# Kernel optimization log

Hardware: AMD Instinct MI355X
Metric: run time of the kernel (lower is better)

Reference implementation:

```python
import jax, jax.numpy as jnp
import numpy as np

B, I, H, OH = 16384, 256, 256, 64
N_STEPS = 8  # fixed-step dopri5 (adaptive step control replaced by fixed grid for jit)


def setup_inputs() -> dict:
    key = jax.random.key(0)
    ks = jax.random.split(key, 12)
    sH = 1.0 / np.sqrt(H)
    sOH = 1.0 / np.sqrt(OH)
    u = lambda k, shape, s: jax.random.uniform(k, shape, jnp.float32, -s, s)
    return {
        "input": jax.random.normal(ks[0], (B, I), jnp.float32),
        "h_prev": jax.random.normal(ks[1], (B, H), jnp.float32),
        "c_prev": jax.random.normal(ks[2], (B, H), jnp.float32),
        "timespans": jax.random.uniform(ks[3], (B,), jnp.float32, 0.05, 1.0),
        # LSTMCell params (PyTorch layout: gates stacked as [i, f, g, o])
        "W_ih": u(ks[4], (4 * H, I), sH),
        "W_hh": u(ks[5], (4 * H, H), sH),
        "b_ih": u(ks[6], (4 * H,), sH),
        "b_hh": u(ks[7], (4 * H,), sH),
        # ode_func: Linear(H, OH) -> Tanh -> Linear(OH, H)
        "W1": u(ks[8], (OH, H), sH),
        "b1": u(ks[9], (OH,), sH),
        "W2": u(ks[10], (H, OH), sOH),
        "b2": u(ks[11], (H,), sOH),
    }


def reference(input, h_prev, c_prev, timespans, W_ih, W_hh, b_ih, b_hh, W1, b1, W2, b2):
    # --- LSTMCell ---
    gates = input @ W_ih.T + b_ih + h_prev @ W_hh.T + b_hh  # (B, 4H)
    gi, gf, gg, go = jnp.split(gates, 4, axis=-1)
    i = jax.nn.sigmoid(gi)
    f = jax.nn.sigmoid(gf)
    g = jnp.tanh(gg)
    o = jax.nn.sigmoid(go)
    c = f * c_prev + i * g
    h = o * jnp.tanh(c)

    # --- Neural ODE: dy/dt = MLP(y), autonomous, Dormand-Prince RK45 ---
    def ode_f(y):
        return jnp.tanh(y @ W1.T + b1) @ W2.T + b2

    dt = (timespans / N_STEPS)[:, None]  # (B, 1) per-sample step size

    def dopri5_step(y, _):
        k1 = ode_f(y)
        k2 = ode_f(y + dt * (1.0 / 5.0 * k1))
        k3 = ode_f(y + dt * (3.0 / 40.0 * k1 + 9.0 / 40.0 * k2))
        k4 = ode_f(y + dt * (44.0 / 45.0 * k1 - 56.0 / 15.0 * k2 + 32.0 / 9.0 * k3))
        k5 = ode_f(y + dt * (19372.0 / 6561.0 * k1 - 25360.0 / 2187.0 * k2
                             + 64448.0 / 6561.0 * k3 - 212.0 / 729.0 * k4))
        k6 = ode_f(y + dt * (9017.0 / 3168.0 * k1 - 355.0 / 33.0 * k2
                             + 46732.0 / 5247.0 * k3 + 49.0 / 176.0 * k4
                             - 5103.0 / 18656.0 * k5))
        y_next = y + dt * (35.0 / 384.0 * k1 + 500.0 / 1113.0 * k3 + 125.0 / 192.0 * k4
                           - 2187.0 / 6784.0 * k5 + 11.0 / 84.0 * k6)
        return y_next, None

    h_ode, _ = jax.lax.scan(dopri5_step, h, None, length=N_STEPS)
    return h_ode, c
```

## Files before the change

### kernel.cpp

```cpp
#include <hip/hip_runtime.h>
#include <hip/hip_bf16.h>


#define B_N 16384
#define H_N 256

typedef __attribute__((ext_vector_type(8))) short short8;
typedef __attribute__((ext_vector_type(4))) unsigned short u16x4;
typedef __attribute__((ext_vector_type(4))) float f32x4;

__device__ __forceinline__ unsigned short f2bf_s(float x) {
  __hip_bfloat16 h = __float2bfloat16(x);
  return *reinterpret_cast<unsigned short*>(&h);
}

__device__ __forceinline__ short8 pack8f(const float* p) {
  const f32x4 a = *(const f32x4*)p;
  const f32x4 b = *(const f32x4*)(p + 4);
  short8 r;
  r[0] = (short)f2bf_s(a[0]); r[1] = (short)f2bf_s(a[1]);
  r[2] = (short)f2bf_s(a[2]); r[3] = (short)f2bf_s(a[3]);
  r[4] = (short)f2bf_s(b[0]); r[5] = (short)f2bf_s(b[1]);
  r[6] = (short)f2bf_s(b[2]); r[7] = (short)f2bf_s(b[3]);
  return r;
}

__device__ __forceinline__ short8 pack8v(f32x4 a, f32x4 b) {
  short8 r;
  r[0] = (short)f2bf_s(a[0]); r[1] = (short)f2bf_s(a[1]);
  r[2] = (short)f2bf_s(a[2]); r[3] = (short)f2bf_s(a[3]);
  r[4] = (short)f2bf_s(b[0]); r[5] = (short)f2bf_s(b[1]);
  r[6] = (short)f2bf_s(b[2]); r[7] = (short)f2bf_s(b[3]);
  return r;
}

__device__ __forceinline__ float fast_sigmoid(float x) {
  return __builtin_amdgcn_rcpf(1.f + __expf(-x));
}
__device__ __forceinline__ float fast_tanh(float x) {
  float e = __expf(2.f * x);
  return 1.f - 2.f * __builtin_amdgcn_rcpf(e + 1.f);
}

__device__ __forceinline__ void gl_lds16(const void* g, void* l) {
  __builtin_amdgcn_global_load_lds(
      (const __attribute__((address_space(1))) void*)g,
      (__attribute__((address_space(3))) void*)l, 16, 0, 0);
}

__global__ __launch_bounds__(256) void prep_kernel(
    const float* __restrict__ Wih, const float* __restrict__ Whh,
    const float* __restrict__ W1, const float* __restrict__ W2,
    const float* __restrict__ b2,
    unsigned short* __restrict__ wsB, unsigned short* __restrict__ wcB,
    float* __restrict__ uF, unsigned short* __restrict__ w1B,
    unsigned short* __restrict__ w2B) {
  const int bx = blockIdx.x;
  if (bx < 256) {
    int idx = bx * 256 + threadIdx.x;
    int n = idx >> 6, c = idx & 63, k = c * 8;
    const float* src = (k < 256) ? (Wih + (size_t)n * 256 + k)
                                 : (Whh + (size_t)n * 256 + (k - 256));
    *(short8*)(wsB + (size_t)n * 512 + k) = pack8f(src);
  } else if (bx < 272) {
    int idx = (bx - 256) * 256 + threadIdx.x;
    int f = idx >> 6, o = idx & 63;
    float a0 = 0.f, a1 = 0.f, a2 = 0.f, a3 = 0.f;
    for (int h = 0; h < 256; h += 4) {
      a0 = fmaf(W1[f * 256 + h],     W2[h * 64 + o],        a0);
      a1 = fmaf(W1[f * 256 + h + 1], W2[(h + 1) * 64 + o],  a1);
      a2 = fmaf(W1[f * 256 + h + 2], W2[(h + 2) * 64 + o],  a2);
      a3 = fmaf(W1[f * 256 + h + 3], W2[(h + 3) * 64 + o],  a3);
    }
    wcB[f * 64 + o] = f2bf_s((a0 + a1) + (a2 + a3));
  } else if (bx == 272) {
    int f = threadIdx.x;
    if (f < 64) {
      float a0 = 0.f, a1 = 0.f, a2 = 0.f, a3 = 0.f;
      for (int h = 0; h < 256; h += 4) {
        a0 = fmaf(W1[f * 256 + h],     b2[h],     a0);
        a1 = fmaf(W1[f * 256 + h + 1], b2[h + 1], a1);
        a2 = fmaf(W1[f * 256 + h + 2], b2[h + 2], a2);
        a3 = fmaf(W1[f * 256 + h + 3], b2[h + 3], a3);
      }
      uF[f] = (a0 + a1) + (a2 + a3);
    }
  } else if (bx < 281) {
    int idx = (bx - 273) * 256 + threadIdx.x;
    *(short8*)(w1B + (size_t)idx * 8) = pack8f(W1 + (size_t)idx * 8);
  } else {
    int idx = (bx - 281) * 256 + threadIdx.x;
    *(short8*)(w2B + (size_t)idx * 8) = pack8f(W2 + (size_t)idx * 8);
  }
}

__global__ __launch_bounds__(512, 4) void lstm_kernel(
    const float* __restrict__ x, const float* __restrict__ hp,
    const float* __restrict__ cp, const unsigned short* __restrict__ wsB,
    const float* __restrict__ bih, const float* __restrict__ bhh,
    float* __restrict__ out) {
  __shared__ __align__(16) unsigned short Abf[2][128 * 32];
  __shared__ __align__(16) unsigned short Bbf[2][256 * 32];

  const int tid = threadIdx.x;
  const int lane = tid & 63;
  const int wv = tid >> 6;
  const int rg = wv >> 2;
  const int cg = wv & 3;
  const int s = lane & 15, q = lane >> 4;
  const int mb = blockIdx.x * 128;
  const int hb = blockIdx.y;

  f32x4 acc[4][4];
#pragma unroll
  for (int mt = 0; mt < 4; ++mt)
#pragma unroll
    for (int g = 0; g < 4; ++g) acc[mt][g] = (f32x4){0.f, 0.f, 0.f, 0.f};

  const int rA = tid >> 2, q4 = tid & 3;
  const int physA = q4 ^ ((rA >> 1) & 3);

  for (int kt = 0; kt < 8; ++kt) {
    const float* srcA = (kt < 4) ? x : hp;
    const int kl = (kt * 64) & 255;

#pragma unroll
    for (int u = 0; u < 2; ++u)
#pragma unroll
      for (int j = 0; j < 2; ++j) {
        int c = wv * 32 + j * 16 + (lane >> 2);
        int lc = (lane & 3) ^ ((c >> 1) & 3);
        int n = (c >> 6) * 256 + hb * 64 + (c & 63);
        gl_lds16(wsB + (size_t)n * 512 + kt * 64 + u * 32 + lc * 8,
                 (char*)Bbf[u] + (wv * 32 + j * 16) * 64);
      }
#pragma unroll
    for (int u = 0; u < 2; ++u) {
      const float* ap = srcA + (size_t)(mb + rA) * 256 + kl + u * 32 + q4 * 8;
      f32x4 v0 = *(const f32x4*)ap;
      f32x4 v1 = *(const f32x4*)(ap + 4);
      *(short8*)((char*)Abf[u] + rA * 64 + physA * 16) = pack8v(v0, v1);
    }
    __syncthreads();

#pragma unroll
    for (int u = 0; u < 2; ++u) {
      short8 af[4];
#pragma unroll
      for (int mt = 0; mt < 4; ++mt) {
        int r = rg * 64 + mt * 16 + s;
        af[mt] = *(const short8*)((char*)Abf[u] + r * 64 +
                                  ((q ^ ((r >> 1) & 3)) << 4));
      }
#pragma unroll
      for (int g = 0; g < 4; ++g) {
        int c = (g * 4 + cg) * 16 + s;
        short8 bfr = *(const short8*)((char*)Bbf[u] + c * 64 +
                                      ((q ^ ((c >> 1) & 3)) << 4));
#pragma unroll
        for (int mt = 0; mt < 4; ++mt)
          acc[mt][g] =
              __builtin_amdgcn_mfma_f32_16x16x32_bf16(af[mt], bfr, acc[mt][g], 0, 0, 0);
      }
    }
    __syncthreads();
  }

#pragma unroll
  for (int mt = 0; mt < 4; ++mt)
#pragma unroll
    for (int r = 0; r < 4; ++r) {
      int sample = mb + rg * 64 + mt * 16 + q * 4 + r;
      int h = hb * 64 + cg * 16 + s;
      float gi = acc[mt][0][r] + bih[h] + bhh[h];
      float gf = acc[mt][1][r] + bih[256 + h] + bhh[256 + h];
      float gg = acc[mt][2][r] + bih[512 + h] + bhh[512 + h];
      float go = acc[mt][3][r] + bih[768 + h] + bhh[768 + h];
      float iv = fast_sigmoid(gi), fv = fast_sigmoid(gf);
      float gv = fast_tanh(gg), ov = fast_sigmoid(go);
      float c = fv * cp[(size_t)sample * 256 + h] + iv * gv;
      float hv = ov * fast_tanh(c);
      out[(size_t)B_N * H_N + (size_t)sample * 256 + h] = c;
      out[(size_t)sample * 256 + h] = hv;
    }
}

__global__ __launch_bounds__(64) void ode_kernel(
    float* __restrict__ out, const float* __restrict__ ts,
    const unsigned short* __restrict__ wcB, const float* __restrict__ uF,
    const unsigned short* __restrict__ w1B, const unsigned short* __restrict__ w2B,
    const float* __restrict__ b1, const float* __restrict__ b2) {
  const int lane = threadIdx.x;
  const int s = lane & 15, q = lane >> 4;
  const int bb = blockIdx.x * 16;

  auto grow = [&](int i) {
    return (i >> 1) * 32 + ((s >> 2) * 8) + (i & 1) * 4 + (s & 3);
  };
  auto fbase = [&](int i) { return (i >> 1) * 32 + q * 8 + (i & 1) * 4; };

  short8 wcf[4][2];
#pragma unroll
  for (int i = 0; i < 4; ++i) {
    const int gr = grow(i);
#pragma unroll
    for (int kt = 0; kt < 2; ++kt)
      wcf[i][kt] = *(const short8*)(wcB + (size_t)gr * 64 + kt * 32 + q * 8);
  }
  f32x4 b1v[4], u4[4];
#pragma unroll
  for (int i = 0; i < 4; ++i) {
    b1v[i] = *(const f32x4*)(b1 + fbase(i));
    u4[i] = *(const f32x4*)(uF + fbase(i));
  }
  const float dt = ts[bb + s] * 0.125f;

  f32x4 G[4];
#pragma unroll
  for (int i = 0; i < 4; ++i) G[i] = (f32x4){0.f, 0.f, 0.f, 0.f};
#pragma unroll
  for (int kt = 0; kt < 8; ++kt) {
    short8 yf = pack8f(out + (size_t)(bb + s) * 256 + kt * 32 + q * 8);
#pragma unroll
    for (int i = 0; i < 4; ++i) {
      short8 w1f =
          *(const short8*)(w1B + (size_t)grow(i) * 256 + kt * 32 + q * 8);
      G[i] = __builtin_amdgcn_mfma_f32_16x16x32_bf16(w1f, yf, G[i], 0, 0, 0);
    }
  }
#pragma unroll
  for (int i = 0; i < 4; ++i) G[i] += b1v[i];

  auto wcmm = [&](const f32x4 (&zc)[4], f32x4 (&o)[4]) {
    short8 zf0 = pack8v(zc[0], zc[1]);
    short8 zf1 = pack8v(zc[2], zc[3]);
#pragma unroll
    for (int i = 0; i < 4; ++i) {
      f32x4 a = (f32x4){0.f, 0.f, 0.f, 0.f};
      a = __builtin_amdgcn_mfma_f32_16x16x32_bf16(wcf[i][0], zf0, a, 0, 0, 0);
      a = __builtin_amdgcn_mfma_f32_16x16x32_bf16(wcf[i][1], zf1, a, 0, 0, 0);
      o[i] = a;
    }
  };
  auto stage = [&](const f32x4 (&zc)[4], float cj, f32x4 (&zo)[4]) {
    f32x4 o[4];
    wcmm(zc, o);
#pragma unroll
    for (int i = 0; i < 4; ++i)
#pragma unroll
      for (int r = 0; r < 4; ++r)
        zo[i][r] = fast_tanh(fmaf(dt, fmaf(cj, u4[i][r], o[i][r]), G[i][r]));
  };

  const float A31 = 3.f / 40.f, A32 = 9.f / 40.f;
  const float A41 = 44.f / 45.f, A42 = -56.f / 15.f, A43 = 32.f / 9.f;
  const float A51 = 19372.f / 6561.f, A52 = -25360.f / 2187.f,
              A53 = 64448.f / 6561.f, A54 = -212.f / 729.f;
  const float A61 = 9017.f / 3168.f, A62 = -355.f / 33.f, A63 = 46732.f / 5247.f,
              A64 = 49.f / 176.f, A65 = -5103.f / 18656.f;
  const float C1 = 35.f / 384.f, C3 = 500.f / 1113.f, C4 = 125.f / 192.f,
              C5 = -2187.f / 6784.f, C6 = 11.f / 84.f;

  f32x4 SC[4];
#pragma unroll
  for (int i = 0; i < 4; ++i) SC[i] = (f32x4){0.f, 0.f, 0.f, 0.f};
  f32x4 z1[4], z2[4], z3[4], z4[4], z5[4], zc[4];

  for (int st = 0; st < 8; ++st) {
#pragma unroll
    for (int i = 0; i < 4; ++i)
#pragma unroll
      for (int r = 0; r < 4; ++r) z1[i][r] = fast_tanh(G[i][r]);

#pragma unroll
    for (int i = 0; i < 4; ++i) zc[i] = 0.2f * z1[i];
    stage(zc, 0.2f, z2);
#pragma unroll
    for (int i = 0; i < 4; ++i) zc[i] = A31 * z1[i] + A32 * z2[i];
    stage(zc, 0.3f, z3);
#pragma unroll
    for (int i = 0; i < 4; ++i) zc[i] = A41 * z1[i] + A42 * z2[i] + A43 * z3[i];
    stage(zc, 0.8f, z4);
#pragma unroll
    for (int i = 0; i < 4; ++i)
      zc[i] = A51 * z1[i] + A52 * z2[i] + A53 * z3[i] + A54 * z4[i];
    stage(zc, 8.f / 9.f, z5);
#pragma unroll
    for (int i = 0; i < 4; ++i)
      zc[i] = A61 * z1[i] + A62 * z2[i] + A63 * z3[i] + A64 * z4[i] + A65 * z5[i];
    {
      f32x4 o[4];
      wcmm(zc, o);
#pragma unroll
      for (int i = 0; i < 4; ++i)
#pragma unroll
        for (int r = 0; r < 4; ++r) {
          float z6v = fast_tanh(fmaf(dt, u4[i][r] + o[i][r], G[i][r]));
          zc[i][r] = C1 * z1[i][r] + C3 * z3[i][r] + C4 * z4[i][r] +
                     C5 * z5[i][r] + C6 * z6v;
        }
    }
    {
      f32x4 o6[4];
      wcmm(zc, o6);
#pragma unroll
      for (int i = 0; i < 4; ++i) {
        SC[i] += zc[i];
#pragma unroll
        for (int r = 0; r < 4; ++r)
          G[i][r] = fmaf(dt, u4[i][r] + o6[i][r], G[i][r]);
      }
    }
  }

  {
    short8 sf0 = pack8v(SC[0], SC[1]);
    short8 sf1 = pack8v(SC[2], SC[3]);
#pragma unroll
    for (int ft = 0; ft < 16; ++ft) {
      short8 w2a = *(const short8*)(w2B + (size_t)(ft * 16 + s) * 64 + q * 8);
      short8 w2b = *(const short8*)(w2B + (size_t)(ft * 16 + s) * 64 + 32 + q * 8);
      f32x4 a = (f32x4){0.f, 0.f, 0.f, 0.f};
      a = __builtin_amdgcn_mfma_f32_16x16x32_bf16(w2a, sf0, a, 0, 0, 0);
      a = __builtin_amdgcn_mfma_f32_16x16x32_bf16(w2b, sf1, a, 0, 0, 0);
      f32x4 y0 = *(const f32x4*)(out + (size_t)(bb + s) * 256 + ft * 16 + q * 4);
      f32x4 b2v = *(const f32x4*)(b2 + ft * 16 + q * 4);
#pragma unroll
      for (int r = 0; r < 4; ++r)
        y0[r] = fmaf(dt, fmaf(8.f, b2v[r], a[r]), y0[r]);
      *(f32x4*)(out + (size_t)(bb + s) * 256 + ft * 16 + q * 4) = y0;
    }
  }
}

extern "C" void kernel_launch(void* const* d_in, const int* in_sizes, int n_in,
                              void* d_out, int out_size, void* d_ws, size_t ws_size,
                              hipStream_t stream) {
  const float* x   = (const float*)d_in[0];
  const float* hp  = (const float*)d_in[1];
  const float* cp  = (const float*)d_in[2];
  const float* ts  = (const float*)d_in[3];
  const float* Wih = (const float*)d_in[4];
  const float* Whh = (const float*)d_in[5];
  const float* bih = (const float*)d_in[6];
  const float* bhh = (const float*)d_in[7];
  const float* W1  = (const float*)d_in[8];
  const float* b1  = (const float*)d_in[9];
  const float* W2  = (const float*)d_in[10];
  const float* b2  = (const float*)d_in[11];
  float* out = (float*)d_out;

  unsigned short* wsB = (unsigned short*)d_ws;
  unsigned short* wcB = (unsigned short*)((char*)d_ws + 1048576);
  float* uF = (float*)((char*)d_ws + 1048576 + 8192);
  unsigned short* w1B = (unsigned short*)((char*)d_ws + 1048576 + 16384);
  unsigned short* w2B = (unsigned short*)((char*)d_ws + 1048576 + 49152);

  prep_kernel<<<289, 256, 0, stream>>>(Wih, Whh, W1, W2, b2, wsB, wcB, uF, w1B, w2B);
  lstm_kernel<<<dim3(128, 4), 512, 0, stream>>>(x, hp, cp, wsB, bih, bhh, out);
  ode_kernel<<<1024, 64, 0, stream>>>(out, ts, wcB, uF, w1B, w2B, b1, b2);
}
```

Measured before the change: 78.41 us.

## Split ODE kernel hidden features across two waves with LDS exchange

The ODE kernel now runs two wavefronts per 16-sample block. Each wave owns half of the 64 hidden ODE features and half of the final output columns. Before each stage matmul the two waves swap their bf16-packed stage vectors through double-buffered shared memory with a block barrier. This halves the serial per-wave MFMA and transcendental work, at the cost of a barrier and LDS round trip at every RK stage.

```diff
diff --git a/kernel.cpp b/kernel.cpp
--- a/kernel.cpp
+++ b/kernel.cpp
@@ -185,71 +185,81 @@
     }
 }
 
-__global__ __launch_bounds__(64) void ode_kernel(
+__global__ __launch_bounds__(128) void ode_kernel(
     float* __restrict__ out, const float* __restrict__ ts,
     const unsigned short* __restrict__ wcB, const float* __restrict__ uF,
     const unsigned short* __restrict__ w1B, const unsigned short* __restrict__ w2B,
     const float* __restrict__ b1, const float* __restrict__ b2) {
-  const int lane = threadIdx.x;
+  __shared__ __align__(16) unsigned short xch[2][2][16 * 4 * 8];
+
+  const int tid = threadIdx.x;
+  const int lane = tid & 63;
+  const int w = tid >> 6;
   const int s = lane & 15, q = lane >> 4;
   const int bb = blockIdx.x * 16;
-
-  auto grow = [&](int i) {
-    return (i >> 1) * 32 + ((s >> 2) * 8) + (i & 1) * 4 + (s & 3);
-  };
-  auto fbase = [&](int i) { return (i >> 1) * 32 + q * 8 + (i & 1) * 4; };
-
-  short8 wcf[4][2];
-#pragma unroll
-  for (int i = 0; i < 4; ++i) {
-    const int gr = grow(i);
+  const int slot = (s * 4 + q) * 8;
+
+  short8 wcf[2][2];
+#pragma unroll
+  for (int j = 0; j < 2; ++j) {
+    const int gr = w * 32 + ((s >> 2) * 8) + j * 4 + (s & 3);
 #pragma unroll
     for (int kt = 0; kt < 2; ++kt)
-      wcf[i][kt] = *(const short8*)(wcB + (size_t)gr * 64 + kt * 32 + q * 8);
-  }
-  f32x4 b1v[4], u4[4];
-#pragma unroll
-  for (int i = 0; i < 4; ++i) {
-    b1v[i] = *(const f32x4*)(b1 + fbase(i));
-    u4[i] = *(const f32x4*)(uF + fbase(i));
+      wcf[j][kt] = *(const short8*)(wcB + (size_t)gr * 64 + kt * 32 + q * 8);
+  }
+  f32x4 b1v[2], u4[2];
+#pragma unroll
+  for (int j = 0; j < 2; ++j) {
+    b1v[j] = *(const f32x4*)(b1 + w * 32 + q * 8 + j * 4);
+    u4[j] = *(const f32x4*)(uF + w * 32 + q * 8 + j * 4);
   }
   const float dt = ts[bb + s] * 0.125f;
 
-  f32x4 G[4];
-#pragma unroll
-  for (int i = 0; i < 4; ++i) G[i] = (f32x4){0.f, 0.f, 0.f, 0.f};
+  f32x4 G[2];
+#pragma unroll
+  for (int j = 0; j < 2; ++j) G[j] = (f32x4){0.f, 0.f, 0.f, 0.f};
 #pragma unroll
   for (int kt = 0; kt < 8; ++kt) {
     short8 yf = pack8f(out + (size_t)(bb + s) * 256 + kt * 32 + q * 8);
 #pragma unroll
-    for (int i = 0; i < 4; ++i) {
-      short8 w1f =
-          *(const short8*)(w1B + (size_t)grow(i) * 256 + kt * 32 + q * 8);
-      G[i] = __builtin_amdgcn_mfma_f32_16x16x32_bf16(w1f, yf, G[i], 0, 0, 0);
-    }
-  }
-#pragma unroll
-  for (int i = 0; i < 4; ++i) G[i] += b1v[i];
-
-  auto wcmm = [&](const f32x4 (&zc)[4], f32x4 (&o)[4]) {
-    short8 zf0 = pack8v(zc[0], zc[1]);
-    short8 zf1 = pack8v(zc[2], zc[3]);
-#pragma unroll
-    for (int i = 0; i < 4; ++i) {
+    for (int j = 0; j < 2; ++j) {
+      const int gr = w * 32 + ((s >> 2) * 8) + j * 4 + (s & 3);
+      short8 w1f = *(const short8*)(w1B + (size_t)gr * 256 + kt * 32 + q * 8);
+      G[j] = __builtin_amdgcn_mfma_f32_16x16x32_bf16(w1f, yf, G[j], 0, 0, 0);
+    }
+  }
+#pragma unroll
+  for (int j = 0; j < 2; ++j) G[j] += b1v[j];
+
+  int buf = 0;
+  auto exch = [&](const f32x4 (&zc)[2], short8& zf0, short8& zf1) {
+    short8 own = pack8v(zc[0], zc[1]);
+    *(short8*)(&xch[buf][w][slot]) = own;
+    __syncthreads();
+    short8 oth = *(const short8*)(&xch[buf][1 - w][slot]);
+    zf0 = w ? oth : own;
+    zf1 = w ? own : oth;
+    buf ^= 1;
+  };
+  auto wcmm = [&](short8 zf0, short8 zf1, f32x4 (&o)[2]) {
+#pragma unroll
+    for (int j = 0; j < 2; ++j) {
       f32x4 a = (f32x4){0.f, 0.f, 0.f, 0.f};
-      a = __builtin_amdgcn_mfma_f32_16x16x32_bf16(wcf[i][0], zf0, a, 0, 0, 0);
-      a = __builtin_amdgcn_mfma_f32_16x16x32_bf16(wcf[i][1], zf1, a, 0, 0, 0);
-      o[i] = a;
+      a = __builtin_amdgcn_mfma_f32_16x16x32_bf16(wcf[j][0], zf0, a, 0, 0, 0);
+      a = __builtin_amdgcn_mfma_f32_16x16x32_bf16(wcf[j][1], zf1, a, 0, 0, 0);
+      o[j] = a;
     }
   };
-  auto stage = [&](const f32x4 (&zc)[4], float cj, f32x4 (&zo)[4]) {
-    f32x4 o[4];
-    wcmm(zc, o);
-#pragma unroll
-    for (int i = 0; i < 4; ++i)
+  auto stage = [&](const f32x4 (&zc)[2], float cj, f32x4 (&zo)[2]) {
+    short8 zf0, zf1;
+    exch(zc, zf0, zf1);
+    f32x4 o[2];
+    wcmm(zf0, zf1, o);
+#pragma unroll
+    for (int j = 0; j < 2; ++j)
 #pragma unroll
       for (int r = 0; r < 4; ++r)
-        zo[i][r] = fast_tanh(fmaf(dt, fmaf(cj, u4[i][r], o[i][r]), G[i][r]));
+        zo[j][r] = fast_tanh(fmaf(dt, fmaf(cj, u4[j][r], o[j][r]), G[j][r]));
   };
 
   const float A31 = 3.f / 40.f, A32 = 9.f / 40.f;
@@ -261,74 +271,79 @@
   const float C1 = 35.f / 384.f, C3 = 500.f / 1113.f, C4 = 125.f / 192.f,
               C5 = -2187.f / 6784.f, C6 = 11.f / 84.f;
 
-  f32x4 SC[4];
-#pragma unroll
-  for (int i = 0; i < 4; ++i) SC[i] = (f32x4){0.f, 0.f, 0.f, 0.f};
-  f32x4 z1[4], z2[4], z3[4], z4[4], z5[4], zc[4];
+  f32x4 SC[2];
+#pragma unroll
+  for (int j = 0; j < 2; ++j) SC[j] = (f32x4){0.f, 0.f, 0.f, 0.f};
+  f32x4 z1[2], z2[2], z3[2], z4[2], z5[2], zc[2];
 
   for (int st = 0; st < 8; ++st) {
 #pragma unroll
-    for (int i = 0; i < 4; ++i)
-#pragma unroll
-      for (int r = 0; r < 4; ++r) z1[i][r] = fast_tanh(G[i][r]);
-
-#pragma unroll
-    for (int i = 0; i < 4; ++i) zc[i] = 0.2f * z1[i];
+    for (int j = 0; j < 2; ++j)
+#pragma unroll
+      for (int r = 0; r < 4; ++r) z1[j][r] = fast_tanh(G[j][r]);
+
+#pragma unroll
+    for (int j = 0; j < 2; ++j) zc[j] = 0.2f * z1[j];
     stage(zc, 0.2f, z2);
 #pragma unroll
-    for (int i = 0; i < 4; ++i) zc[i] = A31 * z1[i] + A32 * z2[i];
+    for (int j = 0; j < 2; ++j) zc[j] = A31 * z1[j] + A32 * z2[j];
     stage(zc, 0.3f, z3);
 #pragma unroll
-    for (int i = 0; i < 4; ++i) zc[i] = A41 * z1[i] + A42 * z2[i] + A43 * z3[i];
+    for (int j = 0; j < 2; ++j) zc[j] = A41 * z1[j] + A42 * z2[j] + A43 * z3[j];
     stage(zc, 0.8f, z4);
 #pragma unroll
-    for (int i = 0; i < 4; ++i)
-      zc[i] = A51 * z1[i] + A52 * z2[i] + A53 * z3[i] + A54 * z4[i];
+    for (int j = 0; j < 2; ++j)
+      zc[j] = A51 * z1[j] + A52 * z2[j] + A53 * z3[j] + A54 * z4[j];
     stage(zc, 8.f / 9.f, z5);
 #pragma unroll
-    for (int i = 0; i < 4; ++i)
-      zc[i] = A61 * z1[i] + A62 * z2[i] + A63 * z3[i] + A64 * z4[i] + A65 * z5[i];
+    for (int j = 0; j < 2; ++j)
+      zc[j] = A61 * z1[j] + A62 * z2[j] + A63 * z3[j] + A64 * z4[j] + A65 * z5[j];
     {
-      f32x4 o[4];
-      wcmm(zc, o);
-#pragma unroll
-      for (int i = 0; i < 4; ++i)
+      short8 zf0, zf1;
+      exch(zc, zf0, zf1);
+      f32x4 o[2];
+      wcmm(zf0, zf1, o);
+#pragma unroll
+      for (int j = 0; j < 2; ++j)
 #pragma unroll
         for (int r = 0; r < 4; ++r) {
-          float z6v = fast_tanh(fmaf(dt, u4[i][r] + o[i][r], G[i][r]));
-          zc[i][r] = C1 * z1[i][r] + C3 * z3[i][r] + C4 * z4[i][r] +
-                     C5 * z5[i][r] + C6 * z6v;
+          float z6v = fast_tanh(fmaf(dt, u4[j][r] + o[j][r], G[j][r]));
+          zc[j][r] = C1 * z1[j][r] + C3 * z3[j][r] + C4 * z4[j][r] +
+                     C5 * z5[j][r] + C6 * z6v;
         }
     }
     {
-      f32x4 o6[4];
-      wcmm(zc, o6);
-#pragma unroll
-      for (int i = 0; i < 4; ++i) {
-        SC[i] += zc[i];
+      short8 zf0, zf1;
+      exch(zc, zf0, zf1);
+      f32x4 o6[2];
+      wcmm(zf0, zf1, o6);
+#pragma unroll
+      for (int j = 0; j < 2; ++j) {
+        SC[j] += zc[j];
 #pragma unroll
         for (int r = 0; r < 4; ++r)
-          G[i][r] = fmaf(dt, u4[i][r] + o6[i][r], G[i][r]);
+          G[j][r] = fmaf(dt, u4[j][r] + o6[j][r], G[j][r]);
       }
     }
   }
 
   {
-    short8 sf0 = pack8v(SC[0], SC[1]);
-    short8 sf1 = pack8v(SC[2], SC[3]);
-#pragma unroll
-    for (int ft = 0; ft < 16; ++ft) {
-      short8 w2a = *(const short8*)(w2B + (size_t)(ft * 16 + s) * 64 + q * 8);
-      short8 w2b = *(const short8*)(w2B + (size_t)(ft * 16 + s) * 64 + 32 + q * 8);
+    short8 sf0, sf1;
+    exch(SC, sf0, sf1);
+#pragma unroll
+    for (int ft = 0; ft < 8; ++ft) {
+      const int f = w * 8 + ft;
+      short8 w2a = *(const short8*)(w2B + (size_t)(f * 16 + s) * 64 + q * 8);
+      short8 w2b = *(const short8*)(w2B + (size_t)(f * 16 + s) * 64 + 32 + q * 8);
       f32x4 a = (f32x4){0.f, 0.f, 0.f, 0.f};
       a = __builtin_amdgcn_mfma_f32_16x16x32_bf16(w2a, sf0, a, 0, 0, 0);
       a = __builtin_amdgcn_mfma_f32_16x16x32_bf16(w2b, sf1, a, 0, 0, 0);
-      f32x4 y0 = *(const f32x4*)(out + (size_t)(bb + s) * 256 + ft * 16 + q * 4);
-      f32x4 b2v = *(const f32x4*)(b2 + ft * 16 + q * 4);
+      f32x4 y0 = *(const f32x4*)(out + (size_t)(bb + s) * 256 + f * 16 + q * 4);
+      f32x4 b2v = *(const f32x4*)(b2 + f * 16 + q * 4);
 #pragma unroll
       for (int r = 0; r < 4; ++r)
         y0[r] = fmaf(dt, fmaf(8.f, b2v[r], a[r]), y0[r]);
-      *(f32x4*)(out + (size_t)(bb + s) * 256 + ft * 16 + q * 4) = y0;
+      *(f32x4*)(out + (size_t)(bb + s) * 256 + f * 16 + q * 4) = y0;
     }
   }
 }
@@ -358,5 +373,5 @@
 
   prep_kernel<<<289, 256, 0, stream>>>(Wih, Whh, W1, W2, b2, wsB, wcB, uF, w1B, w2B);
   lstm_kernel<<<dim3(128, 4), 512, 0, stream>>>(x, hp, cp, wsB, bih, bhh, out);
-  ode_kernel<<<1024, 64, 0, stream>>>(out, ts, wcB, uF, w1B, w2B, b1, b2);
-}
+  ode_kernel<<<1024, 128, 0, stream>>>(out, ts, wcB, uF, w1B, w2B, b1, b2);
+}
```

New measurement: 82.90 us. +5.7%, slower.

## Apply Wc per stage and prescale pre-activations by 2/ln2 for exp2 tanh

Applied to the files above, without the earlier changes.

Restructures the dopri5 stage maths so the small Wc matmul is applied to each stage's tanh output once, and stage inputs are formed as linear combinations of the stored matmul outputs instead of re-multiplying combined z vectors. The final update reuses these w_k results, which removes the extra matmul per step. Pre-activations are kept scaled by 2/ln2 so tanh becomes exp2 plus a reciprocal with no multiply, and the two MFMAs per tile now run independently and are summed instead of chained. The trade-off is more live registers (six w arrays) and a small change in bf16 rounding order.

```diff
diff --git a/kernel.cpp b/kernel.cpp
--- a/kernel.cpp
+++ b/kernel.cpp
@@ -39,6 +39,10 @@
 }
 __device__ __forceinline__ float fast_tanh(float x) {
   float e = __expf(2.f * x);
+  return 1.f - 2.f * __builtin_amdgcn_rcpf(e + 1.f);
+}
+__device__ __forceinline__ float tanh_s(float a2) {
+  float e = exp2f(a2);
   return 1.f - 2.f * __builtin_amdgcn_rcpf(e + 1.f);
 }
 
@@ -207,17 +211,17 @@
     for (int kt = 0; kt < 2; ++kt)
       wcf[i][kt] = *(const short8*)(wcB + (size_t)gr * 64 + kt * 32 + q * 8);
   }
-  f32x4 b1v[4], u4[4];
-#pragma unroll
-  for (int i = 0; i < 4; ++i) {
-    b1v[i] = *(const f32x4*)(b1 + fbase(i));
-    u4[i] = *(const f32x4*)(uF + fbase(i));
-  }
+  f32x4 u4[4];
+#pragma unroll
+  for (int i = 0; i < 4; ++i) u4[i] = *(const f32x4*)(uF + fbase(i));
+
+  const float K2 = 2.8853900817779268f;
   const float dt = ts[bb + s] * 0.125f;
-
-  f32x4 G[4];
-#pragma unroll
-  for (int i = 0; i < 4; ++i) G[i] = (f32x4){0.f, 0.f, 0.f, 0.f};
+  const float dt2 = dt * K2;
+
+  f32x4 G2[4];
+#pragma unroll
+  for (int i = 0; i < 4; ++i) G2[i] = (f32x4){0.f, 0.f, 0.f, 0.f};
 #pragma unroll
   for (int kt = 0; kt < 8; ++kt) {
     short8 yf = pack8f(out + (size_t)(bb + s) * 256 + kt * 32 + q * 8);
@@ -225,31 +229,26 @@
     for (int i = 0; i < 4; ++i) {
       short8 w1f =
           *(const short8*)(w1B + (size_t)grow(i) * 256 + kt * 32 + q * 8);
-      G[i] = __builtin_amdgcn_mfma_f32_16x16x32_bf16(w1f, yf, G[i], 0, 0, 0);
-    }
-  }
-#pragma unroll
-  for (int i = 0; i < 4; ++i) G[i] += b1v[i];
+      G2[i] = __builtin_amdgcn_mfma_f32_16x16x32_bf16(w1f, yf, G2[i], 0, 0, 0);
+    }
+  }
+#pragma unroll
+  for (int i = 0; i < 4; ++i) {
+    f32x4 b1v = *(const f32x4*)(b1 + fbase(i));
+#pragma unroll
+    for (int r = 0; r < 4; ++r) G2[i][r] = (G2[i][r] + b1v[r]) * K2;
+  }
 
   auto wcmm = [&](const f32x4 (&zc)[4], f32x4 (&o)[4]) {
     short8 zf0 = pack8v(zc[0], zc[1]);
     short8 zf1 = pack8v(zc[2], zc[3]);
 #pragma unroll
     for (int i = 0; i < 4; ++i) {
-      f32x4 a = (f32x4){0.f, 0.f, 0.f, 0.f};
-      a = __builtin_amdgcn_mfma_f32_16x16x32_bf16(wcf[i][0], zf0, a, 0, 0, 0);
-      a = __builtin_amdgcn_mfma_f32_16x16x32_bf16(wcf[i][1], zf1, a, 0, 0, 0);
-      o[i] = a;
-    }
-  };
-  auto stage = [&](const f32x4 (&zc)[4], float cj, f32x4 (&zo)[4]) {
-    f32x4 o[4];
-    wcmm(zc, o);
-#pragma unroll
-    for (int i = 0; i < 4; ++i)
-#pragma unroll
-      for (int r = 0; r < 4; ++r)
-        zo[i][r] = fast_tanh(fmaf(dt, fmaf(cj, u4[i][r], o[i][r]), G[i][r]));
+      f32x4 zero = (f32x4){0.f, 0.f, 0.f, 0.f};
+      f32x4 a0 = __builtin_amdgcn_mfma_f32_16x16x32_bf16(wcf[i][0], zf0, zero, 0, 0, 0);
+      f32x4 a1 = __builtin_amdgcn_mfma_f32_16x16x32_bf16(wcf[i][1], zf1, zero, 0, 0, 0);
+      o[i] = a0 + a1;
+    }
   };
 
   const float A31 = 3.f / 40.f, A32 = 9.f / 40.f;
@@ -260,57 +259,83 @@
               A64 = 49.f / 176.f, A65 = -5103.f / 18656.f;
   const float C1 = 35.f / 384.f, C3 = 500.f / 1113.f, C4 = 125.f / 192.f,
               C5 = -2187.f / 6784.f, C6 = 11.f / 84.f;
+  const float c3n = 0.3f, c4n = 0.8f, c5n = 8.f / 9.f;
 
   f32x4 SC[4];
 #pragma unroll
   for (int i = 0; i < 4; ++i) SC[i] = (f32x4){0.f, 0.f, 0.f, 0.f};
-  f32x4 z1[4], z2[4], z3[4], z4[4], z5[4], zc[4];
+  f32x4 z[4], w1[4], w2[4], w3[4], w4[4], w5[4], w6[4], o[4];
 
   for (int st = 0; st < 8; ++st) {
 #pragma unroll
     for (int i = 0; i < 4; ++i)
 #pragma unroll
-      for (int r = 0; r < 4; ++r) z1[i][r] = fast_tanh(G[i][r]);
-
-#pragma unroll
-    for (int i = 0; i < 4; ++i) zc[i] = 0.2f * z1[i];
-    stage(zc, 0.2f, z2);
-#pragma unroll
-    for (int i = 0; i < 4; ++i) zc[i] = A31 * z1[i] + A32 * z2[i];
-    stage(zc, 0.3f, z3);
-#pragma unroll
-    for (int i = 0; i < 4; ++i) zc[i] = A41 * z1[i] + A42 * z2[i] + A43 * z3[i];
-    stage(zc, 0.8f, z4);
-#pragma unroll
-    for (int i = 0; i < 4; ++i)
-      zc[i] = A51 * z1[i] + A52 * z2[i] + A53 * z3[i] + A54 * z4[i];
-    stage(zc, 8.f / 9.f, z5);
-#pragma unroll
-    for (int i = 0; i < 4; ++i)
-      zc[i] = A61 * z1[i] + A62 * z2[i] + A63 * z3[i] + A64 * z4[i] + A65 * z5[i];
-    {
-      f32x4 o[4];
-      wcmm(zc, o);
-#pragma unroll
-      for (int i = 0; i < 4; ++i)
-#pragma unroll
-        for (int r = 0; r < 4; ++r) {
-          float z6v = fast_tanh(fmaf(dt, u4[i][r] + o[i][r], G[i][r]));
-          zc[i][r] = C1 * z1[i][r] + C3 * z3[i][r] + C4 * z4[i][r] +
-                     C5 * z5[i][r] + C6 * z6v;
-        }
-    }
-    {
-      f32x4 o6[4];
-      wcmm(zc, o6);
-#pragma unroll
-      for (int i = 0; i < 4; ++i) {
-        SC[i] += zc[i];
-#pragma unroll
-        for (int r = 0; r < 4; ++r)
-          G[i][r] = fmaf(dt, u4[i][r] + o6[i][r], G[i][r]);
-      }
-    }
+      for (int r = 0; r < 4; ++r) {
+        z[i][r] = tanh_s(G2[i][r]);
+        SC[i][r] = fmaf(C1, z[i][r], SC[i][r]);
+      }
+    wcmm(z, w1);
+#pragma unroll
+    for (int i = 0; i < 4; ++i)
+#pragma unroll
+      for (int r = 0; r < 4; ++r)
+        z[i][r] = tanh_s(fmaf(dt2, 0.2f * (u4[i][r] + w1[i][r]), G2[i][r]));
+    wcmm(z, w2);
+#pragma unroll
+    for (int i = 0; i < 4; ++i)
+#pragma unroll
+      for (int r = 0; r < 4; ++r) {
+        float ov = fmaf(A31, w1[i][r], fmaf(A32, w2[i][r], c3n * u4[i][r]));
+        z[i][r] = tanh_s(fmaf(dt2, ov, G2[i][r]));
+        SC[i][r] = fmaf(C3, z[i][r], SC[i][r]);
+      }
+    wcmm(z, w3);
+#pragma unroll
+    for (int i = 0; i < 4; ++i)
+#pragma unroll
+      for (int r = 0; r < 4; ++r) {
+        float ov = fmaf(A41, w1[i][r],
+                        fmaf(A42, w2[i][r], fmaf(A43, w3[i][r], c4n * u4[i][r])));
+        z[i][r] = tanh_s(fmaf(dt2, ov, G2[i][r]));
+        SC[i][r] = fmaf(C4, z[i][r], SC[i][r]);
+      }
+    wcmm(z, w4);
+#pragma unroll
+    for (int i = 0; i < 4; ++i)
+#pragma unroll
+      for (int r = 0; r < 4; ++r) {
+        float ov = fmaf(A51, w1[i][r],
+                        fmaf(A52, w2[i][r],
+                             fmaf(A53, w3[i][r],
+                                  fmaf(A54, w4[i][r], c5n * u4[i][r]))));
+        z[i][r] = tanh_s(fmaf(dt2, ov, G2[i][r]));
+        SC[i][r] = fmaf(C5, z[i][r], SC[i][r]);
+      }
+    wcmm(z, w5);
+#pragma unroll
+    for (int i = 0; i < 4; ++i)
+#pragma unroll
+      for (int r = 0; r < 4; ++r) {
+        float ov = fmaf(A61, w1[i][r],
+                        fmaf(A62, w2[i][r],
+                             fmaf(A63, w3[i][r],
+                                  fmaf(A64, w4[i][r],
+                                       fmaf(A65, w5[i][r], u4[i][r])))));
+        z[i][r] = tanh_s(fmaf(dt2, ov, G2[i][r]));
+        SC[i][r] = fmaf(C6, z[i][r], SC[i][r]);
+      }
+    wcmm(z, w6);
+#pragma unroll
+    for (int i = 0; i < 4; ++i)
+#pragma unroll
+      for (int r = 0; r < 4; ++r) {
+        float ov = fmaf(C1, w1[i][r],
+                        fmaf(C3, w3[i][r],
+                             fmaf(C4, w4[i][r],
+                                  fmaf(C5, w5[i][r],
+                                       fmaf(C6, w6[i][r], u4[i][r])))));
+        G2[i][r] = fmaf(dt2, ov, G2[i][r]);
+      }
   }
 
   {
@@ -320,14 +345,14 @@
     for (int ft = 0; ft < 16; ++ft) {
       short8 w2a = *(const short8*)(w2B + (size_t)(ft * 16 + s) * 64 + q * 8);
       short8 w2b = *(const short8*)(w2B + (size_t)(ft * 16 + s) * 64 + 32 + q * 8);
-      f32x4 a = (f32x4){0.f, 0.f, 0.f, 0.f};
-      a = __builtin_amdgcn_mfma_f32_16x16x32_bf16(w2a, sf0, a, 0, 0, 0);
-      a = __builtin_amdgcn_mfma_f32_16x16x32_bf16(w2b, sf1, a, 0, 0, 0);
+      f32x4 zero = (f32x4){0.f, 0.f, 0.f, 0.f};
+      f32x4 a0 = __builtin_amdgcn_mfma_f32_16x16x32_bf16(w2a, sf0, zero, 0, 0, 0);
+      f32x4 a1 = __builtin_amdgcn_mfma_f32_16x16x32_bf16(w2b, sf1, zero, 0, 0, 0);
       f32x4 y0 = *(const f32x4*)(out + (size_t)(bb + s) * 256 + ft * 16 + q * 4);
       f32x4 b2v = *(const f32x4*)(b2 + ft * 16 + q * 4);
 #pragma unroll
       for (int r = 0; r < 4; ++r)
-        y0[r] = fmaf(dt, fmaf(8.f, b2v[r], a[r]), y0[r]);
+        y0[r] = fmaf(dt, fmaf(8.f, b2v[r], a0[r] + a1[r]), y0[r]);
       *(f32x4*)(out + (size_t)(bb + s) * 256 + ft * 16 + q * 4) = y0;
     }
   }
```

New measurement: 85.61 us. +9.2%, slower.

## Double-buffer LSTM gate GEMM K-loop to overlap loads with MFMA

Applied to the files above, without the earlier changes.

Restructures the LSTM gate GEMM main loop from 8 K-steps of 64, each with two sub-buffers, into 16 K-steps of 32 with ping-pong LDS buffers. The next tile's weights are prefetched via global-to-LDS loads and the next A tile into registers while MFMAs run on the current buffer. This leaves one barrier per step instead of two. It aims to hide global load latency behind compute, at the cost of more loop iterations and held prefetch registers.

```diff
diff --git a/kernel.cpp b/kernel.cpp
--- a/kernel.cpp
+++ b/kernel.cpp
@@ -120,49 +120,61 @@
   const int rA = tid >> 2, q4 = tid & 3;
   const int physA = q4 ^ ((rA >> 1) & 3);
 
-  for (int kt = 0; kt < 8; ++kt) {
-    const float* srcA = (kt < 4) ? x : hp;
-    const int kl = (kt * 64) & 255;
-
-#pragma unroll
-    for (int u = 0; u < 2; ++u)
-#pragma unroll
-      for (int j = 0; j < 2; ++j) {
-        int c = wv * 32 + j * 16 + (lane >> 2);
-        int lc = (lane & 3) ^ ((c >> 1) & 3);
-        int n = (c >> 6) * 256 + hb * 64 + (c & 63);
-        gl_lds16(wsB + (size_t)n * 512 + kt * 64 + u * 32 + lc * 8,
-                 (char*)Bbf[u] + (wv * 32 + j * 16) * 64);
-      }
-#pragma unroll
-    for (int u = 0; u < 2; ++u) {
-      const float* ap = srcA + (size_t)(mb + rA) * 256 + kl + u * 32 + q4 * 8;
-      f32x4 v0 = *(const f32x4*)ap;
-      f32x4 v1 = *(const f32x4*)(ap + 4);
-      *(short8*)((char*)Abf[u] + rA * 64 + physA * 16) = pack8v(v0, v1);
-    }
-    __syncthreads();
-
-#pragma unroll
-    for (int u = 0; u < 2; ++u) {
-      short8 af[4];
-#pragma unroll
-      for (int mt = 0; mt < 4; ++mt) {
-        int r = rg * 64 + mt * 16 + s;
-        af[mt] = *(const short8*)((char*)Abf[u] + r * 64 +
-                                  ((q ^ ((r >> 1) & 3)) << 4));
-      }
-#pragma unroll
-      for (int g = 0; g < 4; ++g) {
-        int c = (g * 4 + cg) * 16 + s;
-        short8 bfr = *(const short8*)((char*)Bbf[u] + c * 64 +
-                                      ((q ^ ((c >> 1) & 3)) << 4));
-#pragma unroll
-        for (int mt = 0; mt < 4; ++mt)
-          acc[mt][g] =
-              __builtin_amdgcn_mfma_f32_16x16x32_bf16(af[mt], bfr, acc[mt][g], 0, 0, 0);
-      }
-    }
+  auto BSTAGE = [&](int kt, int p) {
+#pragma unroll
+    for (int j = 0; j < 2; ++j) {
+      int c16 = wv * 2 + j;
+      int row = c16 * 16 + (lane >> 2);
+      int lc = (lane & 3) ^ ((row >> 1) & 3);
+      int n = (row >> 6) * 256 + hb * 64 + (row & 63);
+      gl_lds16(wsB + (size_t)n * 512 + kt * 32 + lc * 8,
+               (char*)Bbf[p] + c16 * 1024);
+    }
+  };
+
+  f32x4 pa0, pa1;
+  auto ALOAD = [&](int kt) {
+    const float* srcA = (kt < 8) ? x : hp;
+    const int kl = (kt * 32) & 255;
+    const float* ap = srcA + (size_t)(mb + rA) * 256 + kl + q4 * 8;
+    pa0 = *(const f32x4*)ap;
+    pa1 = *(const f32x4*)(ap + 4);
+  };
+  auto AWRITE = [&](int p) {
+    *(short8*)((char*)Abf[p] + rA * 64 + physA * 16) = pack8v(pa0, pa1);
+  };
+
+  BSTAGE(0, 0);
+  ALOAD(0);
+  AWRITE(0);
+  __syncthreads();
+
+  for (int kt = 0; kt < 16; ++kt) {
+    const int p = kt & 1;
+    if (kt < 15) {
+      BSTAGE(kt + 1, p ^ 1);
+      ALOAD(kt + 1);
+    }
+
+    short8 af[4];
+#pragma unroll
+    for (int mt = 0; mt < 4; ++mt) {
+      int r = rg * 64 + mt * 16 + s;
+      af[mt] = *(const short8*)((char*)Abf[p] + r * 64 +
+                                ((q ^ ((r >> 1) & 3)) << 4));
+    }
+#pragma unroll
+    for (int g = 0; g < 4; ++g) {
+      int c = (g * 4 + cg) * 16 + s;
+      short8 bfr = *(const short8*)((char*)Bbf[p] + c * 64 +
+                                    ((q ^ ((c >> 1) & 3)) << 4));
+#pragma unroll
+      for (int mt = 0; mt < 4; ++mt)
+        acc[mt][g] =
+            __builtin_amdgcn_mfma_f32_16x16x32_bf16(af[mt], bfr, acc[mt][g], 0, 0, 0);
+    }
+
+    if (kt < 15) AWRITE(p ^ 1);
     __syncthreads();
   }
 
```

After: 77.22 us (median of 2 runs). About the same (-1.5%).
